# Kernel tuning notes

Measured on AMD Instinct MI355X. Metric: run time of the kernel, lower is better.

Reference implementation:

```python
import jax, jax.numpy as jnp
import numpy as np
from jax import lax

EPS = 1e-5

def setup_inputs() -> dict:
    key = jax.random.key(0)
    ks = jax.random.split(key, 8)
    B, D, H, W = 2, 96, 96, 96
    K, N, R = 4, 16, 6
    return {
        "x": jax.random.normal(ks[0], (B, D, H, W), jnp.float32),
        "x_proj_weight": jax.random.normal(ks[1], (K, R + 2 * N, D), jnp.float32) * 0.05,
        "dt_projs_weight": jax.random.normal(ks[2], (K, D, R), jnp.float32) * 0.05,
        "dt_projs_bias": jax.random.normal(ks[3], (K, D), jnp.float32) * 0.05,
        "A_logs": jax.random.uniform(ks[4], (K * D, N), jnp.float32, 0.0, 1.0),
        "Ds": jax.random.normal(ks[5], (K * D,), jnp.float32) * 0.1,
        "norm_weight": jnp.ones((D,), jnp.float32),
        "norm_bias": jnp.zeros((D,), jnp.float32),
    }

def _cross_scan(x):
    # x: [B,C,H,W] -> xs: [B,4,C,L]; dirs: row-major, col-major, and their flips
    B, C, H, W = x.shape
    x_hw = x.reshape(B, C, H * W)
    x_wh = jnp.swapaxes(x, 2, 3).reshape(B, C, H * W)
    return jnp.stack([x_hw, x_wh, x_hw[..., ::-1], x_wh[..., ::-1]], axis=1)

def _cross_merge(ys, H, W):
    # ys: [B,4,C,L] -> y: [B,C,L]
    B, K, C, L = ys.shape
    ys = ys[:, 0:2] + ys[:, 2:4][..., ::-1]
    y_wh = jnp.swapaxes(ys[:, 1].reshape(B, C, W, H), 2, 3).reshape(B, C, L)
    return ys[:, 0] + y_wh

def _forward(x, x_proj_weight, dt_projs_weight, dt_projs_bias, A_logs, Ds,
             norm_weight, norm_bias):
    B, D, H, W = x.shape
    L = H * W
    K, _, R = dt_projs_weight.shape
    N = A_logs.shape[1]

    xs = _cross_scan(x)                                        # [B,K,D,L]
    x_dbl = jnp.einsum('bkdl,kcd->bkcl', xs, x_proj_weight)    # [B,K,R+2N,L]
    dts, Bs, Cs = x_dbl[:, :, :R], x_dbl[:, :, R:R + N], x_dbl[:, :, R + N:]
    dts = jnp.einsum('bkrl,kdr->bkdl', dts, dt_projs_weight)   # [B,K,D,L]

    A = -jnp.exp(A_logs).reshape(K, D, N)                      # [K,D,N]
    delta = jax.nn.softplus(dts + dt_projs_bias[None, :, :, None])  # [B,K,D,L]

    # time-major for scan
    u_t = jnp.moveaxis(xs, 3, 0)       # [L,B,K,D]
    d_t = jnp.moveaxis(delta, 3, 0)    # [L,B,K,D]
    B_t = jnp.moveaxis(Bs, 3, 0)       # [L,B,K,N]
    C_t = jnp.moveaxis(Cs, 3, 0)       # [L,B,K,N]

    def step(h, inp):
        u, dlt, b, c = inp
        h = jnp.exp(dlt[..., None] * A) * h + (dlt * u)[..., None] * b[:, :, None, :]
        y = jnp.einsum('bkdn,bkn->bkd', h, c)
        return h, y

    h0 = jnp.zeros((B, K, D, N), xs.dtype)
    _, ys = lax.scan(step, h0, (u_t, d_t, B_t, C_t))           # ys: [L,B,K,D]
    ys = jnp.moveaxis(ys, 0, 3)                                # [B,K,D,L]
    ys = ys + Ds.reshape(1, K, D, 1) * xs                      # skip term

    y = _cross_merge(ys, H, W)                                 # [B,D,L]
    y = jnp.swapaxes(y, 1, 2)                                  # [B,L,D]
    # out_norm: LayerNorm over channel dim
    mu = y.mean(-1, keepdims=True)
    var = y.var(-1, keepdims=True)
    y = (y - mu) / jnp.sqrt(var + EPS) * norm_weight + norm_bias
    return y.reshape(B, H, W, D)

def reference(x, x_proj_weight, dt_projs_weight, dt_projs_bias, A_logs, Ds,
              norm_weight, norm_bias):
    return _forward(x, x_proj_weight, dt_projs_weight, dt_projs_bias,
                    A_logs, Ds, norm_weight, norm_bias)
```

## Files before the change

kernel.cpp:

```cpp
#include <hip/hip_runtime.h>
#include <hip/hip_bf16.h>
#include <hip/hip_fp16.h>


constexpr int Bn = 2, Kn = 4, Dn = 96, Hn = 96, Wn = 96, Ln = Hn * Wn;
constexpr int Nn = 16, Rn = 6;
constexpr int CCn = 288, CLn = 32;

#define DI __device__ __forceinline__

typedef _Float16 half2v __attribute__((ext_vector_type(2)));

DI float bf2f(unsigned short u) { return __uint_as_float(((unsigned)u) << 16); }
DI bool probe_bf16(const void* nw) { return ((const unsigned*)nw)[0] == 0x3F803F80u; }
DI float ld_in(const void* p, long i, bool bf) {
  return bf ? bf2f(((const unsigned short*)p)[i]) : ((const float*)p)[i];
}
DI float fexp2(float x) {
#if __has_builtin(__builtin_amdgcn_exp2f)
  return __builtin_amdgcn_exp2f(x);
#else
  return exp2f(x);
#endif
}
DI float softplus_fast(float v) {
  return (v > 15.f) ? v : __logf(1.f + __expf(v));
}
DI float dot2acc(unsigned a, unsigned b, float c) {
#if __has_builtin(__builtin_amdgcn_fdot2)
  half2v av, bv;
  __builtin_memcpy(&av, &a, 4);
  __builtin_memcpy(&bv, &b, 4);
  return __builtin_amdgcn_fdot2(av, bv, c, false);
#else
  __half2 ah = *(__half2*)&a, bh = *(__half2*)&b;
  float2 af = __half22float2(ah), bf2_ = __half22float2(bh);
  return fmaf(af.y, bf2_.y, fmaf(af.x, bf2_.x, c));
#endif
}
DI float quad_reduce_add(float v) {
  int a = __builtin_amdgcn_mov_dpp(__float_as_int(v), 0xB1, 0xF, 0xF, true);
  v += __int_as_float(a);
  int b = __builtin_amdgcn_mov_dpp(__float_as_int(v), 0x4E, 0xF, 0xF, true);
  v += __int_as_float(b);
  return v;
}
constexpr float LOG2E = 1.44269504088896340736f;

__global__ __launch_bounds__(256) void k_prep(
    const void* __restrict__ x, const void* __restrict__ xpw,
    const void* __restrict__ dtw, const void* __restrict__ dtb,
    const void* __restrict__ Al, const void* __restrict__ Ds,
    const void* __restrict__ nw, const void* __restrict__ nb,
    float* __restrict__ xl, float* __restrict__ xlT,
    __half* __restrict__ wp_h, unsigned* __restrict__ wdt_p,
    float* __restrict__ bias_f, float* __restrict__ Al_f,
    float* __restrict__ dsum, float* __restrict__ nw_f, float* __restrict__ nb_f) {
  __shared__ float tile[96 * 97];
  bool bf = probe_bf16(nw);
  int h = blockIdx.x, b = blockIdx.y;
  int tid = threadIdx.x;
  int fi = (blockIdx.y * gridDim.x + blockIdx.x) * 256 + tid;
  int fgs = gridDim.x * gridDim.y * 256;
  for (int i = fi; i < Kn * 4000; i += fgs) {
    int k = i / 4000, r = i - k * 4000;
    int c = r / 100, dd = r - c * 100;
    wp_h[i] = __float2half(
        (c < 38 && dd < 96) ? ld_in(xpw, (long)k * 38 * 96 + c * 96 + dd, bf)
                            : 0.f);
  }
  for (int i = fi; i < Kn * Dn; i += fgs) {
    float r01a = ld_in(dtw, (long)i * 6 + 0, bf);
    float r01b = ld_in(dtw, (long)i * 6 + 1, bf);
    float r23a = ld_in(dtw, (long)i * 6 + 2, bf);
    float r23b = ld_in(dtw, (long)i * 6 + 3, bf);
    float r45a = ld_in(dtw, (long)i * 6 + 4, bf);
    float r45b = ld_in(dtw, (long)i * 6 + 5, bf);
    __half2 h01 = __floats2half2_rn(r01a, r01b);
    __half2 h23 = __floats2half2_rn(r23a, r23b);
    __half2 h45 = __floats2half2_rn(r45a, r45b);
    wdt_p[i * 4 + 0] = *(unsigned*)&h01;
    wdt_p[i * 4 + 1] = *(unsigned*)&h23;
    wdt_p[i * 4 + 2] = *(unsigned*)&h45;
    wdt_p[i * 4 + 3] = 0u;
    bias_f[i] = ld_in(dtb, i, bf);
  }
  for (int i = fi; i < Kn * Dn * Nn; i += fgs)
    Al_f[i] = -__expf(ld_in(Al, i, bf)) * LOG2E;
  for (int i = fi; i < Dn; i += fgs) {
    dsum[i] = ld_in(Ds, i, bf) + ld_in(Ds, 96 + i, bf) +
              ld_in(Ds, 192 + i, bf) + ld_in(Ds, 288 + i, bf);
    nw_f[i] = ld_in(nw, i, bf);
    nb_f[i] = ld_in(nb, i, bf);
  }
  long srcbase = (long)b * Dn * Ln + (long)h * 96;
  for (int i = tid; i < 96 * 96; i += 256) {
    int d = i / 96, w = i - d * 96;
    tile[d * 97 + w] = ld_in(x, srcbase + (long)d * Ln + w, bf);
  }
  __syncthreads();
  float* xlb = xl + (size_t)b * Ln * 96;
  float* xTb = xlT + (size_t)b * Ln * 96;
  for (int i = tid; i < 96 * 96; i += 256) {
    int w = i / 96, d = i - w * 96;
    float v = tile[d * 97 + w];
    xlb[(size_t)(h * 96 + w) * 96 + d] = v;
    xTb[(size_t)(w * 96 + h) * 96 + d] = v;
  }
}

__global__ __launch_bounds__(256) void k_proj(
    const float* __restrict__ xl, const float* __restrict__ xlT,
    const __half* __restrict__ wp_h, const unsigned* __restrict__ wdt_p,
    const float* __restrict__ bias_f, const float* __restrict__ Al_f,
    __half2* __restrict__ ddu, __half* __restrict__ BCh,
    float* __restrict__ PSg) {
  constexpr int TL = 32;
  __shared__ __half xt[TL * 102];
  __shared__ __half wp[40 * 100];
  __shared__ __half xd2[TL * 40];
  __shared__ unsigned wdt_u[96 * 4];
  __shared__ float bias[96];
  int tile = blockIdx.x, k = blockIdx.y, b = blockIdx.z;
  int l0 = tile * TL;
  int tid = threadIdx.x;
  bool rev = (k & 2) != 0;

  {
    const uint4* wsrc = (const uint4*)(wp_h + (size_t)k * 4000);
    for (int i = tid; i < 500; i += 256) ((uint4*)wp)[i] = wsrc[i];
    const uint4* dsrc = (const uint4*)(wdt_p + (size_t)k * 384);
    for (int i = tid; i < 96; i += 256) ((uint4*)wdt_u)[i] = dsrc[i];
    if (tid < 96) bias[tid] = bias_f[k * 96 + tid];
  }
  {
    const float* xsrc = ((k & 1) ? xlT : xl) + (size_t)b * Ln * 96;
    for (int i = tid; i < TL * 24; i += 256) {
      int r = i / 24, q = i - r * 24;
      int g = rev ? (Ln - 1 - l0 - r) : (l0 + r);
      float4 v = *(const float4*)(xsrc + (size_t)g * 96 + q * 4);
      *(__half2*)(&xt[r * 102 + q * 4]) = __floats2half2_rn(v.x, v.y);
      *(__half2*)(&xt[r * 102 + q * 4 + 2]) = __floats2half2_rn(v.z, v.w);
    }
  }
  __syncthreads();

  {
    int jg = tid & 31, cg = tid >> 5;
    int c0 = cg * 5;
    float acc[5] = {0.f, 0.f, 0.f, 0.f, 0.f};
    for (int dd = 0; dd < 96; dd += 4) {
      uint2 xa = *(const uint2*)&xt[jg * 102 + dd];
#pragma unroll
      for (int i = 0; i < 5; ++i) {
        uint2 wv = *(const uint2*)&wp[(c0 + i) * 100 + dd];
        acc[i] = dot2acc(xa.x, wv.x, acc[i]);
        acc[i] = dot2acc(xa.y, wv.y, acc[i]);
      }
    }
#pragma unroll
    for (int i = 0; i < 5; ++i) xd2[jg * 40 + c0 + i] = __float2half(acc[i]);
  }
  __syncthreads();

  size_t bk = (size_t)b * 4 + k;
  {
    __half2* o = (__half2*)(BCh + (bk * (size_t)Ln + l0) * 32);
    for (int i = tid; i < TL * 16; i += 256) {
      int j = i >> 4, cp = i & 15;
      int c = cp * 2;
      int ng = c >> 3, idx = c & 7;
      int ch = (idx < 4) ? (6 + ng * 4 + idx) : (22 + ng * 4 + (idx - 4));
      o[i] = *(const __half2*)&xd2[j * 40 + ch];
    }
  }
  if (tid < 192) {
    int d = tid >> 1, hg = tid & 1;
    unsigned wv0 = wdt_u[d * 4], wv1 = wdt_u[d * 4 + 1], wv2 = wdt_u[d * 4 + 2];
    float bd = bias[d];
    float ac2[8];
    *(float4*)&ac2[0] = *(const float4*)&Al_f[(k * 96 + d) * 16 + hg * 8];
    *(float4*)&ac2[4] = *(const float4*)&Al_f[(k * 96 + d) * 16 + hg * 8 + 4];
    float P[8] = {1.f, 1.f, 1.f, 1.f, 1.f, 1.f, 1.f, 1.f};
    float S[8] = {0.f, 0.f, 0.f, 0.f, 0.f, 0.f, 0.f, 0.f};
    __half2* dcol = ddu + (bk * (size_t)Ln + l0) * 96 + d;
#pragma unroll 2
    for (int t = 0; t < TL; ++t) {
      uint2 xr01 = *(const uint2*)&xd2[t * 40];
      unsigned xr2 = *(const unsigned*)&xd2[t * 40 + 4];
      float v = dot2acc(xr01.x, wv0,
                dot2acc(xr01.y, wv1,
                dot2acc(xr2, wv2, bd)));
      float sp = softplus_fast(v);
      float u = __half2float(xt[t * 102 + d]);
      __half2 pk = __floats2half2_rn(sp, sp * u);
      if (hg == 0) dcol[(size_t)t * 96] = pk;
      float2 pf = __half22float2(pk);
      float spc = pf.x, fy = pf.y;
#pragma unroll
      for (int w = 0; w < 4; ++w) {
        unsigned bw = *(const unsigned*)&xd2[t * 40 + 6 + 8 * hg + 2 * w];
        float2 Bv = __half22float2(*(__half2*)&bw);
        float a0 = fexp2(spc * ac2[w * 2]);
        P[w * 2] *= a0;
        S[w * 2] = fmaf(a0, S[w * 2], fy * Bv.x);
        float a1 = fexp2(spc * ac2[w * 2 + 1]);
        P[w * 2 + 1] *= a1;
        S[w * 2 + 1] = fmaf(a1, S[w * 2 + 1], fy * Bv.y);
      }
    }
    size_t ob = ((size_t)(bk * 96 + d) * CCn + tile) * 32 + hg * 8;
    *(float4*)&PSg[ob] = make_float4(P[0], P[1], P[2], P[3]);
    *(float4*)&PSg[ob + 4] = make_float4(P[4], P[5], P[6], P[7]);
    *(float4*)&PSg[ob + 16] = make_float4(S[0], S[1], S[2], S[3]);
    *(float4*)&PSg[ob + 20] = make_float4(S[4], S[5], S[6], S[7]);
  }
}

__global__ __launch_bounds__(256) void k_midscan(float* __restrict__ PSg) {
  __shared__ float Pl[256], Sl[256];
  int bkd = blockIdx.x;
  int tid = threadIdx.x;
  int g = tid >> 4, n = tid & 15;
  constexpr int CPG = CCn / 16;
  size_t base = ((size_t)bkd * CCn + (size_t)g * CPG) * 32 + n;
  float Pr[CPG], Sr[CPG];
#pragma unroll
  for (int i = 0; i < CPG; ++i) {
    Pr[i] = PSg[base + (size_t)i * 32];
    Sr[i] = PSg[base + (size_t)i * 32 + 16];
  }
  float Pa = 1.f, Sa = 0.f;
#pragma unroll
  for (int i = 0; i < CPG; ++i) { Sa = fmaf(Pr[i], Sa, Sr[i]); Pa *= Pr[i]; }
  Pl[tid] = Pa;
  Sl[tid] = Sa;
  __syncthreads();
#pragma unroll
  for (int s = 1; s < 16; s <<= 1) {
    float Pp = 1.f, Sp = 0.f;
    if (g >= s) { Pp = Pl[(g - s) * 16 + n]; Sp = Sl[(g - s) * 16 + n]; }
    __syncthreads();
    if (g >= s) {
      Sl[tid] = fmaf(Pl[tid], Sp, Sl[tid]);
      Pl[tid] *= Pp;
    }
    __syncthreads();
  }
  float h = (g == 0) ? 0.f : Sl[(g - 1) * 16 + n];
#pragma unroll
  for (int i = 0; i < CPG; ++i) {
    PSg[base + (size_t)i * 32] = h;
    h = fmaf(Pr[i], h, Sr[i]);
  }
}

__global__ __launch_bounds__(192) void k_scan2(
    const __half2* __restrict__ ddu, const __half* __restrict__ BCh,
    const float* __restrict__ Al_f, const float* __restrict__ PSg,
    __half* __restrict__ ysH) {
  __shared__ __half2 dd_s[CLn * 96];
  __shared__ __half bc_s[CLn * 32];
  int chunk = blockIdx.x, k = blockIdx.y, b = blockIdx.z;
  int tid = threadIdx.x;
  int dp = tid >> 2, ng = tid & 3;
  int d0 = dp * 2, n0 = ng * 4;
  int bk = b * 4 + k;
  int t0 = chunk * CLn;
  float ac[2][4];
#pragma unroll
  for (int dd = 0; dd < 2; ++dd)
#pragma unroll
    for (int j = 0; j < 4; ++j)
      ac[dd][j] = Al_f[(k * 96 + d0 + dd) * 16 + n0 + j];
  {
    const uint4* dsrc = (const uint4*)(ddu + ((size_t)bk * Ln + t0) * 96);
    uint4* ddst = (uint4*)dd_s;
    for (int i = tid; i < CLn * 96 / 4; i += 192) ddst[i] = dsrc[i];
    const uint4* bsrc = (const uint4*)(BCh + ((size_t)bk * Ln + t0) * 32);
    uint4* bdst = (uint4*)bc_s;
    for (int i = tid; i < CLn * 32 * 2 / 16; i += 192) bdst[i] = bsrc[i];
  }
  float4 ha = *(const float4*)(PSg + ((size_t)(bk * 96 + d0) * CCn + chunk) * 32 + n0);
  float4 hb = *(const float4*)(PSg + ((size_t)(bk * 96 + d0 + 1) * CCn + chunk) * 32 + n0);
  float h[2][4] = {{ha.x, ha.y, ha.z, ha.w}, {hb.x, hb.y, hb.z, hb.w}};
  __syncthreads();

#pragma unroll 2
  for (int t = 0; t < CLn; ++t) {
    union { uint2 u; __half2 h2[2]; } dv;
    dv.u = *(const uint2*)&dd_s[t * 96 + d0];
    union { uint4 u; __half2 h2[4]; } bc;
    bc.u = *(const uint4*)&bc_s[t * 32 + ng * 8];
    float2 f0 = __half22float2(dv.h2[0]);
    float2 f1 = __half22float2(dv.h2[1]);
    float2 b01 = __half22float2(bc.h2[0]);
    float2 b23 = __half22float2(bc.h2[1]);
    float2 c01 = __half22float2(bc.h2[2]);
    float2 c23 = __half22float2(bc.h2[3]);
    float Ba[4] = {b01.x, b01.y, b23.x, b23.y};
    float Ca[4] = {c01.x, c01.y, c23.x, c23.y};
    float py0 = 0.f, py1 = 0.f;
#pragma unroll
    for (int j = 0; j < 4; ++j) {
      float a0 = fexp2(f0.x * ac[0][j]);
      h[0][j] = fmaf(a0, h[0][j], f0.y * Ba[j]);
      py0 = fmaf(h[0][j], Ca[j], py0);
      float a1 = fexp2(f1.x * ac[1][j]);
      h[1][j] = fmaf(a1, h[1][j], f1.y * Ba[j]);
      py1 = fmaf(h[1][j], Ca[j], py1);
    }
    py0 = quad_reduce_add(py0);
    py1 = quad_reduce_add(py1);
    if (ng == 0)
      *(__half2*)&ysH[((size_t)bk * Ln + t0 + t) * 96 + d0] =
          __halves2half2(__float2half(py0), __float2half(py1));
  }
}

__global__ __launch_bounds__(256) void k_merge_ln(
    const __half* __restrict__ ysH, const float* __restrict__ xl,
    const float* __restrict__ dsum, const void* __restrict__ nwraw,
    const float* __restrict__ nw_f, const float* __restrict__ nb_f,
    void* __restrict__ outv) {
  __shared__ float yt[64 * 98];
  __shared__ float nwf[96], nbf[96], dsm[96], mu_s[64], rs_s[64];
  bool bf = probe_bf16(nwraw);
  int tile = blockIdx.x, b = blockIdx.y;
  int h0 = (tile / 12) * 8, w0 = (tile % 12) * 8;
  int tid = threadIdx.x;
  if (tid < 96) {
    nwf[tid] = nw_f[tid];
    nbf[tid] = nb_f[tid];
    dsm[tid] = dsum[tid];
  }
  const __half* y0 = ysH + (size_t)(b * 4 + 0) * Ln * 96;
  const __half* y1 = ysH + (size_t)(b * 4 + 1) * Ln * 96;
  const __half* y2 = ysH + (size_t)(b * 4 + 2) * Ln * 96;
  const __half* y3 = ysH + (size_t)(b * 4 + 3) * Ln * 96;
  const float* xb = xl + (size_t)b * Ln * 96;
  __syncthreads();
  for (int i = tid; i < 64 * 48; i += 256) {
    int rr = i / 48, dp = i - rr * 48, d = dp * 2;
    int hh = h0 + (rr >> 3), ww = w0 + (rr & 7);
    int l = hh * 96 + ww, t1 = ww * 96 + hh;
    float2 v0 = __half22float2(*(const __half2*)&y0[(size_t)l * 96 + d]);
    float2 v1 = __half22float2(*(const __half2*)&y1[(size_t)t1 * 96 + d]);
    float2 v2 = __half22float2(*(const __half2*)&y2[(size_t)(Ln - 1 - l) * 96 + d]);
    float2 v3 = __half22float2(*(const __half2*)&y3[(size_t)(Ln - 1 - t1) * 96 + d]);
    float2 xv = *(const float2*)&xb[(size_t)l * 96 + d];
    float2 r;
    r.x = v0.x + v1.x + v2.x + v3.x + dsm[d] * xv.x;
    r.y = v0.y + v1.y + v2.y + v3.y + dsm[d + 1] * xv.y;
    *(float2*)&yt[rr * 98 + d] = r;
  }
  __syncthreads();
  {
    int rr = tid >> 2, qq = tid & 3;
    float s = 0.f, ss = 0.f;
#pragma unroll 4
    for (int d2 = 0; d2 < 24; ++d2) {
      float v = yt[rr * 98 + qq * 24 + d2];
      s += v;
      ss += v * v;
    }
    s = quad_reduce_add(s);
    ss = quad_reduce_add(ss);
    if (qq == 0) {
      float mu = s * (1.f / 96.f);
      float var = fmaxf(ss * (1.f / 96.f) - mu * mu, 0.f);
      mu_s[rr] = mu;
      rs_s[rr] = rsqrtf(var + 1e-5f);
    }
  }
  __syncthreads();
  for (int i = tid; i < 64 * 48; i += 256) {
    int rr = i / 48, dp = i - rr * 48, d = dp * 2;
    int hh = h0 + (rr >> 3), ww = w0 + (rr & 7);
    size_t idx = ((size_t)b * Ln + hh * 96 + ww) * 96 + d;
    float2 yv = *(const float2*)&yt[rr * 98 + d];
    float mu = mu_s[rr], rs = rs_s[rr];
    float o0 = (yv.x - mu) * rs * nwf[d] + nbf[d];
    float o1 = (yv.y - mu) * rs * nwf[d + 1] + nbf[d + 1];
    if (bf) {
      union { unsigned u; unsigned short us[2]; } pk;
      __hip_bfloat16 b0 = __float2bfloat16(o0), b1 = __float2bfloat16(o1);
      pk.us[0] = *(unsigned short*)&b0;
      pk.us[1] = *(unsigned short*)&b1;
      *(unsigned*)&((__hip_bfloat16*)outv)[idx] = pk.u;
    } else {
      *(float2*)&((float*)outv)[idx] = make_float2(o0, o1);
    }
  }
}

extern "C" void kernel_launch(void* const* d_in, const int* in_sizes, int n_in,
                              void* d_out, int out_size, void* d_ws, size_t ws_size,
                              hipStream_t stream) {
  const void* x   = d_in[0];
  const void* xpw = d_in[1];
  const void* dtw = d_in[2];
  const void* dtb = d_in[3];
  const void* Al  = d_in[4];
  const void* Ds  = d_in[5];
  const void* nw  = d_in[6];
  const void* nb  = d_in[7];

  char* ws = (char*)d_ws;
  size_t off = 0;
  auto alloc = [&](size_t bytes) {
    char* p = ws + off;
    off += (bytes + 511) & ~(size_t)511;
    return p;
  };
  float* xl    = (float*)alloc((size_t)Bn * Ln * Dn * 4);
  float* xlT   = (float*)alloc((size_t)Bn * Ln * Dn * 4);
  __half* wp_h = (__half*)alloc((size_t)Kn * 4000 * 2);
  unsigned* wdt_p = (unsigned*)alloc((size_t)Kn * Dn * 4 * 4);
  float* bias_f= (float*)alloc((size_t)Kn * Dn * 4);
  float* Al_f  = (float*)alloc((size_t)Kn * Dn * Nn * 4);
  float* dsum  = (float*)alloc((size_t)Dn * 4);
  float* nw_f  = (float*)alloc((size_t)Dn * 4);
  float* nb_f  = (float*)alloc((size_t)Dn * 4);
  __half2* ddu = (__half2*)alloc((size_t)Bn * Kn * Ln * Dn * 4);
  __half* BCh  = (__half*)alloc((size_t)Bn * Kn * Ln * 32 * 2);
  float* PS    = (float*)alloc((size_t)Bn * Kn * Dn * CCn * 32 * 4);
  __half* ysH  = (__half*)alloc((size_t)Bn * Kn * Ln * Dn * 2);
  (void)ws_size; (void)in_sizes; (void)n_in; (void)out_size;

  k_prep<<<dim3(Hn, Bn), dim3(256), 0, stream>>>(
      x, xpw, dtw, dtb, Al, Ds, nw, nb, xl, xlT, wp_h, wdt_p, bias_f, Al_f,
      dsum, nw_f, nb_f);
  k_proj<<<dim3(Ln / 32, Kn, Bn), dim3(256), 0, stream>>>(
      xl, xlT, wp_h, wdt_p, bias_f, Al_f, ddu, BCh, PS);
  k_midscan<<<dim3(Bn * Kn * Dn), dim3(256), 0, stream>>>(PS);
  k_scan2<<<dim3(CCn, Kn, Bn), dim3(192), 0, stream>>>(ddu, BCh, Al_f, PS, ysH);
  k_merge_ln<<<dim3(144, Bn), dim3(256), 0, stream>>>(ysH, xl, dsum, nw, nw_f,
                                                      nb_f, d_out);
}
```

Baseline: 184.4 us.

## Retile prep, projection chunks and merge-LN; compute chunk decay from summed delta

```diff
diff --git a/kernel.cpp b/kernel.cpp
--- a/kernel.cpp
+++ b/kernel.cpp
@@ -5,7 +5,7 @@
 
 constexpr int Bn = 2, Kn = 4, Dn = 96, Hn = 96, Wn = 96, Ln = Hn * Wn;
 constexpr int Nn = 16, Rn = 6;
-constexpr int CCn = 288, CLn = 32;
+constexpr int TLn = 36, CCn = 256, CLn = 36;
 
 #define DI __device__ __forceinline__
 
@@ -56,12 +56,14 @@
     __half* __restrict__ wp_h, unsigned* __restrict__ wdt_p,
     float* __restrict__ bias_f, float* __restrict__ Al_f,
     float* __restrict__ dsum, float* __restrict__ nw_f, float* __restrict__ nb_f) {
-  __shared__ float tile[96 * 97];
+  __shared__ float tile[96 * 49];
   bool bf = probe_bf16(nw);
-  int h = blockIdx.x, b = blockIdx.y;
+  int h = blockIdx.x, wh = blockIdx.y, b = blockIdx.z;
+  int w0 = wh * 48;
   int tid = threadIdx.x;
-  int fi = (blockIdx.y * gridDim.x + blockIdx.x) * 256 + tid;
-  int fgs = gridDim.x * gridDim.y * 256;
+  int fi = ((blockIdx.z * gridDim.y + blockIdx.y) * gridDim.x + blockIdx.x) *
+               256 + tid;
+  int fgs = gridDim.x * gridDim.y * gridDim.z * 256;
   for (int i = fi; i < Kn * 4000; i += fgs) {
     int k = i / 4000, r = i - k * 4000;
     int c = r / 100, dd = r - c * 100;
@@ -70,19 +72,15 @@
                             : 0.f);
   }
   for (int i = fi; i < Kn * Dn; i += fgs) {
-    float r01a = ld_in(dtw, (long)i * 6 + 0, bf);
-    float r01b = ld_in(dtw, (long)i * 6 + 1, bf);
-    float r23a = ld_in(dtw, (long)i * 6 + 2, bf);
-    float r23b = ld_in(dtw, (long)i * 6 + 3, bf);
-    float r45a = ld_in(dtw, (long)i * 6 + 4, bf);
-    float r45b = ld_in(dtw, (long)i * 6 + 5, bf);
-    __half2 h01 = __floats2half2_rn(r01a, r01b);
-    __half2 h23 = __floats2half2_rn(r23a, r23b);
-    __half2 h45 = __floats2half2_rn(r45a, r45b);
-    wdt_p[i * 4 + 0] = *(unsigned*)&h01;
-    wdt_p[i * 4 + 1] = *(unsigned*)&h23;
-    wdt_p[i * 4 + 2] = *(unsigned*)&h45;
-    wdt_p[i * 4 + 3] = 0u;
+    __half2 h01 = __floats2half2_rn(ld_in(dtw, (long)i * 6 + 0, bf),
+                                    ld_in(dtw, (long)i * 6 + 1, bf));
+    __half2 h23 = __floats2half2_rn(ld_in(dtw, (long)i * 6 + 2, bf),
+                                    ld_in(dtw, (long)i * 6 + 3, bf));
+    __half2 h45 = __floats2half2_rn(ld_in(dtw, (long)i * 6 + 4, bf),
+                                    ld_in(dtw, (long)i * 6 + 5, bf));
+    wdt_p[i * 3 + 0] = *(unsigned*)&h01;
+    wdt_p[i * 3 + 1] = *(unsigned*)&h23;
+    wdt_p[i * 3 + 2] = *(unsigned*)&h45;
     bias_f[i] = ld_in(dtb, i, bf);
   }
   for (int i = fi; i < Kn * Dn * Nn; i += fgs)
@@ -93,19 +91,19 @@
     nw_f[i] = ld_in(nw, i, bf);
     nb_f[i] = ld_in(nb, i, bf);
   }
-  long srcbase = (long)b * Dn * Ln + (long)h * 96;
-  for (int i = tid; i < 96 * 96; i += 256) {
-    int d = i / 96, w = i - d * 96;
-    tile[d * 97 + w] = ld_in(x, srcbase + (long)d * Ln + w, bf);
+  long srcbase = (long)b * Dn * Ln + (long)h * 96 + w0;
+  for (int i = tid; i < 96 * 48; i += 256) {
+    int d = i / 48, w = i - d * 48;
+    tile[d * 49 + w] = ld_in(x, srcbase + (long)d * Ln + w, bf);
   }
   __syncthreads();
   float* xlb = xl + (size_t)b * Ln * 96;
   float* xTb = xlT + (size_t)b * Ln * 96;
-  for (int i = tid; i < 96 * 96; i += 256) {
+  for (int i = tid; i < 48 * 96; i += 256) {
     int w = i / 96, d = i - w * 96;
-    float v = tile[d * 97 + w];
-    xlb[(size_t)(h * 96 + w) * 96 + d] = v;
-    xTb[(size_t)(w * 96 + h) * 96 + d] = v;
+    float v = tile[d * 49 + w];
+    xlb[(size_t)(h * 96 + w0 + w) * 96 + d] = v;
+    xTb[(size_t)((w0 + w) * 96 + h) * 96 + d] = v;
   }
 }
 
@@ -115,7 +113,7 @@
     const float* __restrict__ bias_f, const float* __restrict__ Al_f,
     __half2* __restrict__ ddu, __half* __restrict__ BCh,
     float* __restrict__ PSg) {
-  constexpr int TL = 32;
+  constexpr int TL = TLn;
   __shared__ __half xt[TL * 102];
   __shared__ __half wp[40 * 100];
   __shared__ __half xd2[TL * 40];
@@ -129,8 +127,11 @@
   {
     const uint4* wsrc = (const uint4*)(wp_h + (size_t)k * 4000);
     for (int i = tid; i < 500; i += 256) ((uint4*)wp)[i] = wsrc[i];
-    const uint4* dsrc = (const uint4*)(wdt_p + (size_t)k * 384);
-    for (int i = tid; i < 96; i += 256) ((uint4*)wdt_u)[i] = dsrc[i];
+    const unsigned* dsrc = wdt_p + (size_t)k * 288;
+    for (int i = tid; i < 288; i += 256) {
+      int d = i / 3, r = i - d * 3;
+      wdt_u[d * 4 + r] = dsrc[i];
+    }
     if (tid < 96) bias[tid] = bias_f[k * 96 + tid];
   }
   {
@@ -146,20 +147,22 @@
   __syncthreads();
 
   {
-    int jg = tid & 31, cg = tid >> 5;
-    int c0 = cg * 5;
-    float acc[5] = {0.f, 0.f, 0.f, 0.f, 0.f};
-    for (int dd = 0; dd < 96; dd += 4) {
-      uint2 xa = *(const uint2*)&xt[jg * 102 + dd];
-#pragma unroll
-      for (int i = 0; i < 5; ++i) {
-        uint2 wv = *(const uint2*)&wp[(c0 + i) * 100 + dd];
-        acc[i] = dot2acc(xa.x, wv.x, acc[i]);
-        acc[i] = dot2acc(xa.y, wv.y, acc[i]);
+    for (int it = tid; it < TL * 8; it += 256) {
+      int j = it >> 3, cg = it & 7;
+      int c0 = cg * 5;
+      float acc[5] = {0.f, 0.f, 0.f, 0.f, 0.f};
+      for (int dd = 0; dd < 96; dd += 4) {
+        uint2 xa = *(const uint2*)&xt[j * 102 + dd];
+#pragma unroll
+        for (int i = 0; i < 5; ++i) {
+          uint2 wv = *(const uint2*)&wp[(c0 + i) * 100 + dd];
+          acc[i] = dot2acc(xa.x, wv.x, acc[i]);
+          acc[i] = dot2acc(xa.y, wv.y, acc[i]);
+        }
       }
-    }
-#pragma unroll
-    for (int i = 0; i < 5; ++i) xd2[jg * 40 + c0 + i] = __float2half(acc[i]);
+#pragma unroll
+      for (int i = 0; i < 5; ++i) xd2[j * 40 + c0 + i] = __float2half(acc[i]);
+    }
   }
   __syncthreads();
 
@@ -181,7 +184,7 @@
     float ac2[8];
     *(float4*)&ac2[0] = *(const float4*)&Al_f[(k * 96 + d) * 16 + hg * 8];
     *(float4*)&ac2[4] = *(const float4*)&Al_f[(k * 96 + d) * 16 + hg * 8 + 4];
-    float P[8] = {1.f, 1.f, 1.f, 1.f, 1.f, 1.f, 1.f, 1.f};
+    float spsum = 0.f;
     float S[8] = {0.f, 0.f, 0.f, 0.f, 0.f, 0.f, 0.f, 0.f};
     __half2* dcol = ddu + (bk * (size_t)Ln + l0) * 96 + d;
 #pragma unroll 2
@@ -192,23 +195,30 @@
                 dot2acc(xr01.y, wv1,
                 dot2acc(xr2, wv2, bd)));
       float sp = softplus_fast(v);
+      __half sph = __float2half(sp);
+      float spc = __half2float(sph);
       float u = __half2float(xt[t * 102 + d]);
-      __half2 pk = __floats2half2_rn(sp, sp * u);
-      if (hg == 0) dcol[(size_t)t * 96] = pk;
-      float2 pf = __half22float2(pk);
-      float spc = pf.x, fy = pf.y;
+      __half fyh = __float2half(spc * u);
+      float fy = __half2float(fyh);
+      if (hg == 0) dcol[(size_t)t * 96] = __halves2half2(sph, fyh);
+      spsum += spc;
+      unsigned bw0 = *(const unsigned*)&xd2[t * 40 + 6 + hg * 8];
+      unsigned bw1 = *(const unsigned*)&xd2[t * 40 + 8 + hg * 8];
+      unsigned bw2 = *(const unsigned*)&xd2[t * 40 + 10 + hg * 8];
+      unsigned bw3 = *(const unsigned*)&xd2[t * 40 + 12 + hg * 8];
+      unsigned bws[4] = {bw0, bw1, bw2, bw3};
 #pragma unroll
       for (int w = 0; w < 4; ++w) {
-        unsigned bw = *(const unsigned*)&xd2[t * 40 + 6 + 8 * hg + 2 * w];
-        float2 Bv = __half22float2(*(__half2*)&bw);
+        float2 Bv = __half22float2(*(__half2*)&bws[w]);
         float a0 = fexp2(spc * ac2[w * 2]);
-        P[w * 2] *= a0;
         S[w * 2] = fmaf(a0, S[w * 2], fy * Bv.x);
         float a1 = fexp2(spc * ac2[w * 2 + 1]);
-        P[w * 2 + 1] *= a1;
         S[w * 2 + 1] = fmaf(a1, S[w * 2 + 1], fy * Bv.y);
       }
     }
+    float P[8];
+#pragma unroll
+    for (int j = 0; j < 8; ++j) P[j] = fexp2(spsum * ac2[j]);
     size_t ob = ((size_t)(bk * 96 + d) * CCn + tile) * 32 + hg * 8;
     *(float4*)&PSg[ob] = make_float4(P[0], P[1], P[2], P[3]);
     *(float4*)&PSg[ob + 4] = make_float4(P[4], P[5], P[6], P[7]);
@@ -323,11 +333,11 @@
     const float* __restrict__ dsum, const void* __restrict__ nwraw,
     const float* __restrict__ nw_f, const float* __restrict__ nb_f,
     void* __restrict__ outv) {
-  __shared__ float yt[64 * 98];
-  __shared__ float nwf[96], nbf[96], dsm[96], mu_s[64], rs_s[64];
+  __shared__ float yt[32 * 98];
+  __shared__ float nwf[96], nbf[96], dsm[96], mu_s[32], rs_s[32];
   bool bf = probe_bf16(nwraw);
   int tile = blockIdx.x, b = blockIdx.y;
-  int h0 = (tile / 12) * 8, w0 = (tile % 12) * 8;
+  int h0 = (tile / 12) * 4, w0 = (tile % 12) * 8;
   int tid = threadIdx.x;
   if (tid < 96) {
     nwf[tid] = nw_f[tid];
@@ -340,7 +350,7 @@
   const __half* y3 = ysH + (size_t)(b * 4 + 3) * Ln * 96;
   const float* xb = xl + (size_t)b * Ln * 96;
   __syncthreads();
-  for (int i = tid; i < 64 * 48; i += 256) {
+  for (int i = tid; i < 32 * 48; i += 256) {
     int rr = i / 48, dp = i - rr * 48, d = dp * 2;
     int hh = h0 + (rr >> 3), ww = w0 + (rr & 7);
     int l = hh * 96 + ww, t1 = ww * 96 + hh;
@@ -356,16 +366,19 @@
   }
   __syncthreads();
   {
-    int rr = tid >> 2, qq = tid & 3;
+    int rr = tid >> 3, qq = tid & 7;
     float s = 0.f, ss = 0.f;
 #pragma unroll 4
-    for (int d2 = 0; d2 < 24; ++d2) {
-      float v = yt[rr * 98 + qq * 24 + d2];
+    for (int j = 0; j < 12; ++j) {
+      float v = yt[rr * 98 + qq * 12 + j];
       s += v;
       ss += v * v;
     }
-    s = quad_reduce_add(s);
-    ss = quad_reduce_add(ss);
+#pragma unroll
+    for (int m = 1; m < 8; m <<= 1) {
+      s += __shfl_xor(s, m, 64);
+      ss += __shfl_xor(ss, m, 64);
+    }
     if (qq == 0) {
       float mu = s * (1.f / 96.f);
       float var = fmaxf(ss * (1.f / 96.f) - mu * mu, 0.f);
@@ -374,7 +387,7 @@
     }
   }
   __syncthreads();
-  for (int i = tid; i < 64 * 48; i += 256) {
+  for (int i = tid; i < 32 * 48; i += 256) {
     int rr = i / 48, dp = i - rr * 48, d = dp * 2;
     int hh = h0 + (rr >> 3), ww = w0 + (rr & 7);
     size_t idx = ((size_t)b * Ln + hh * 96 + ww) * 96 + d;
@@ -416,7 +429,7 @@
   float* xl    = (float*)alloc((size_t)Bn * Ln * Dn * 4);
   float* xlT   = (float*)alloc((size_t)Bn * Ln * Dn * 4);
   __half* wp_h = (__half*)alloc((size_t)Kn * 4000 * 2);
-  unsigned* wdt_p = (unsigned*)alloc((size_t)Kn * Dn * 4 * 4);
+  unsigned* wdt_p = (unsigned*)alloc((size_t)Kn * Dn * 3 * 4);
   float* bias_f= (float*)alloc((size_t)Kn * Dn * 4);
   float* Al_f  = (float*)alloc((size_t)Kn * Dn * Nn * 4);
   float* dsum  = (float*)alloc((size_t)Dn * 4);
@@ -428,13 +441,13 @@
   __half* ysH  = (__half*)alloc((size_t)Bn * Kn * Ln * Dn * 2);
   (void)ws_size; (void)in_sizes; (void)n_in; (void)out_size;
 
-  k_prep<<<dim3(Hn, Bn), dim3(256), 0, stream>>>(
+  k_prep<<<dim3(Hn, 2, Bn), dim3(256), 0, stream>>>(
       x, xpw, dtw, dtb, Al, Ds, nw, nb, xl, xlT, wp_h, wdt_p, bias_f, Al_f,
       dsum, nw_f, nb_f);
-  k_proj<<<dim3(Ln / 32, Kn, Bn), dim3(256), 0, stream>>>(
+  k_proj<<<dim3(Ln / TLn, Kn, Bn), dim3(256), 0, stream>>>(
       xl, xlT, wp_h, wdt_p, bias_f, Al_f, ddu, BCh, PS);
   k_midscan<<<dim3(Bn * Kn * Dn), dim3(256), 0, stream>>>(PS);
   k_scan2<<<dim3(CCn, Kn, Bn), dim3(192), 0, stream>>>(ddu, BCh, Al_f, PS, ysH);
-  k_merge_ln<<<dim3(144, Bn), dim3(256), 0, stream>>>(ysH, xl, dsum, nw, nw_f,
+  k_merge_ln<<<dim3(288, Bn), dim3(256), 0, stream>>>(ysH, xl, dsum, nw, nw_f,
                                                       nb_f, d_out);
 }
```

Result: slower. 205.6 us (+11.5%).
